# Kernel tuning notes

Measured on AMD Instinct MI355X. Metric: run time of the kernel, lower is better.

Reference implementation:

```python
import jax, jax.numpy as jnp
import numpy as np

B, T_CTX, N_EMBD, N_ATTN, N_HEAD = 8, 1024, 1024, 1024, 16
HEAD_SIZE = N_ATTN // N_HEAD


def _init_time_w():
    # replicates the torch init: per-head exponential decay curves
    curve = np.array([-(T_CTX - 1 - i) for i in range(T_CTX)], dtype=np.float64)
    ww = np.ones((N_HEAD, T_CTX), dtype=np.float32)
    for h in range(N_HEAD):
        if h < N_HEAD - 1:
            decay_speed = T_CTX ** (-(h + 1) / (N_HEAD - 1))
        else:
            decay_speed = 0.0
        ww[h] = np.exp(curve * decay_speed).astype(np.float32)
    return jnp.asarray(ww)


def setup_inputs() -> dict:
    key = jax.random.key(0)
    ks = jax.random.split(key, 6)
    s = 0.02
    return {
        "x": jax.random.normal(ks[0], (B, T_CTX, N_EMBD), jnp.float32),
        "time_w": _init_time_w(),                                   # [H, TT]
        "time_alpha": jnp.ones((N_HEAD, 1, T_CTX), jnp.float32),
        "time_beta": jnp.ones((N_HEAD, T_CTX, 1), jnp.float32),
        "time_gamma": jnp.ones((T_CTX, 1), jnp.float32),
        "Wk": jax.random.normal(ks[1], (N_ATTN, N_EMBD), jnp.float32) * s,
        "bk": jnp.zeros((N_ATTN,), jnp.float32),
        "Wv": jax.random.normal(ks[2], (N_ATTN, N_EMBD), jnp.float32) * s,
        "bv": jnp.zeros((N_ATTN,), jnp.float32),
        "Wr": jax.random.normal(ks[3], (N_ATTN, N_EMBD), jnp.float32) * s,
        "br": jnp.zeros((N_ATTN,), jnp.float32),
        "Wo": jax.random.normal(ks[4], (N_EMBD, N_ATTN), jnp.float32) * s,
        "bo": jnp.zeros((N_EMBD,), jnp.float32),
    }


def _build_w(time_w, time_alpha, time_beta, T):
    # w[h,t,u] = time_w[h, TT-1-(t-u)] for u<=t else 0  (causal decay matrix)
    TT = time_w.shape[1]
    t = jnp.arange(T)[:, None]
    u = jnp.arange(T)[None, :]
    idx = jnp.clip((TT - 1) - t + u, 0, TT - 1)
    mask = u <= t
    w = jnp.where(mask[None, :, :], time_w[:, idx], 0.0)  # [H, T, T]
    return w * time_alpha[:, :, :T] * time_beta[:, :T, :]


def reference(x, time_w, time_alpha, time_beta, time_gamma,
              Wk, bk, Wv, bv, Wr, br, Wo, bo):
    Bb, T, C = x.shape
    H = time_w.shape[0]
    w = _build_w(time_w, time_alpha, time_beta, T)  # [H,T,T]

    # time shift on the first half of channels: prepend zero row, drop last
    x_half = jnp.pad(x[:, :, : C // 2], ((0, 0), (1, 0), (0, 0)))[:, :T, :]
    xs = jnp.concatenate([x_half, x[:, :, C // 2 :]], axis=-1)

    k = xs @ Wk.T + bk
    v = xs @ Wv.T + bv
    r = xs @ Wr.T + br

    k = jnp.exp(jnp.clip(k, -60.0, 30.0))
    sum_k = jnp.cumsum(k, axis=1)  # [B,T,NA]

    kv = (k * v).reshape(Bb, T, H, -1)               # [B,T,H,hs]
    wkv = jnp.einsum('htu,buhc->bthc', w, kv).reshape(Bb, T, -1)

    rwkv = jax.nn.sigmoid(r) * wkv / sum_k
    out = rwkv @ Wo.T + bo
    return out * time_gamma[:T]
```

## Files before the change

kernel.cpp:

```cpp
#include <hip/hip_runtime.h>
#include <hip/hip_bf16.h>
#include <cstddef>
#include <cstdint>

#define B_SZ   8
#define T_CTX  1024
#define C_DIM  1024
#define H_NUM  16
#define HS     64
#define M_ROWS (B_SZ * T_CTX)

typedef __attribute__((ext_vector_type(8))) short bf16x8;
typedef __attribute__((ext_vector_type(8))) unsigned short u16x8;
typedef __attribute__((ext_vector_type(4))) float f32x4;

static __device__ inline unsigned short f2bf(float f) {
    __hip_bfloat16 h = __float2bfloat16(f);
    return __builtin_bit_cast(unsigned short, h);
}
static __device__ inline float bf2f(unsigned short u) {
    unsigned int v = ((unsigned int)u) << 16;
    return __builtin_bit_cast(float, v);
}
static __device__ inline void gld16(const void* g, void* l) {
    __builtin_amdgcn_global_load_lds((const __attribute__((address_space(1))) void*)g,
                                     (__attribute__((address_space(3))) void*)l,
                                     16, 0, 0);
}

__global__ __launch_bounds__(256)
void convert_all(const float* __restrict__ x, unsigned short* __restrict__ xs,
                 const float* __restrict__ Wk, const float* __restrict__ Wv,
                 const float* __restrict__ Wr, const float* __restrict__ Wo,
                 unsigned short* __restrict__ wdst)
{
    const int bid = blockIdx.x;
    if (bid < 8192) {
        const int idx = (bid * 256 + threadIdx.x) * 4;
        const int m = idx >> 10;
        const int c = idx & 1023;
        float4 v;
        if (c < 512) {
            const int t = m & (T_CTX - 1);
            if (t == 0) v = make_float4(0.f, 0.f, 0.f, 0.f);
            else        v = *(const float4*)(x + (size_t)(m - 1) * C_DIM + c);
        } else {
            v = *(const float4*)(x + idx);
        }
        ushort4 o;
        o.x = f2bf(v.x); o.y = f2bf(v.y); o.z = f2bf(v.z); o.w = f2bf(v.w);
        *(ushort4*)(xs + idx) = o;
    } else {
        const int wid = bid - 8192;
        const int z = wid >> 10;
        const float* src = (z == 0) ? Wk : (z == 1) ? Wv : (z == 2) ? Wr : Wo;
        const int idx = ((wid & 1023) * 256 + threadIdx.x) * 4;
        const float4 v = *(const float4*)(src + idx);
        ushort4 o;
        o.x = f2bf(v.x); o.y = f2bf(v.y); o.z = f2bf(v.z); o.w = f2bf(v.w);
        *(ushort4*)(wdst + (size_t)z * (C_DIM * C_DIM) + idx) = o;
    }
}

__global__ __launch_bounds__(256, 2)
void mfma_gemm64(const unsigned short* __restrict__ A,
                 const unsigned short* __restrict__ Wb,
                 const float* __restrict__ b0, const float* __restrict__ b1,
                 const float* __restrict__ b2,
                 void* __restrict__ o0, void* __restrict__ o1, void* __restrict__ o2,
                 const float* __restrict__ gamma, int multi)
{
    const int d  = blockIdx.x;
    const int y  = ((d & 7) << 3) | ((d >> 3) & 7);
    const int xb = d >> 6;
    const int m0 = y * 128, n0 = xb * 128;

    int mode, ncol0;
    const float* bias;
    void* out;
    if (multi) {
        const int z = n0 >> 10;
        mode = z;
        ncol0 = n0 & 1023;
        bias = (z == 0) ? b0 : (z == 1) ? b1 : b2;
        out  = (z == 0) ? o0 : (z == 1) ? o1 : o2;
    } else {
        mode = 3; ncol0 = n0; bias = b0; out = o0;
    }

    __shared__ unsigned short As[128 * 64];
    __shared__ unsigned short Bs[128 * 64];

    const int tid = threadIdx.x;
    const int w = tid >> 6, l = tid & 63;

    const int r8  = l >> 3;
    const int c16 = ((l & 7) ^ r8) * 8;
    const unsigned short* gA = A  + (size_t)(m0 + w * 32 + r8) * C_DIM + c16;
    const unsigned short* gB = Wb + (size_t)(n0 + w * 32 + r8) * C_DIM + c16;
    char* lA = (char*)As + (w * 32) * 128;
    char* lB = (char*)Bs + (w * 32) * 128;

    const int wr = w >> 1, wc = w & 1;
    const int lr = l & 15, lkq = l >> 4;
    const int x7 = lr & 7;

    f32x4 acc[4][4];
    #pragma unroll
    for (int i = 0; i < 4; ++i)
        #pragma unroll
        for (int j = 0; j < 4; ++j) acc[i][j] = (f32x4){0.f, 0.f, 0.f, 0.f};

    for (int k0 = 0; k0 < C_DIM; k0 += 64) {
        #pragma unroll
        for (int r = 0; r < 4; ++r) {
            gld16(gA + k0 + (size_t)r * 8 * C_DIM, lA + r * 8 * 128);
            gld16(gB + k0 + (size_t)r * 8 * C_DIM, lB + r * 8 * 128);
        }
        __syncthreads();

        bf16x8 af[2][4], bfv[2][4];
        #pragma unroll
        for (int ks = 0; ks < 2; ++ks) {
            const int slot = ((ks * 4 + lkq) ^ x7) * 8;
            #pragma unroll
            for (int i = 0; i < 4; ++i)
                af[ks][i] = *(const bf16x8*)&As[(wr * 64 + i * 16 + lr) * 64 + slot];
            #pragma unroll
            for (int j = 0; j < 4; ++j)
                bfv[ks][j] = *(const bf16x8*)&Bs[(wc * 64 + j * 16 + lr) * 64 + slot];
        }
        #pragma unroll
        for (int ks = 0; ks < 2; ++ks)
            #pragma unroll
            for (int i = 0; i < 4; ++i)
                #pragma unroll
                for (int j = 0; j < 4; ++j)
                    acc[i][j] = __builtin_amdgcn_mfma_f32_16x16x32_bf16(
                        af[ks][i], bfv[ks][j], acc[i][j], 0, 0, 0);
        __syncthreads();
    }

    #pragma unroll
    for (int j = 0; j < 4; ++j) {
        const int col = ncol0 + wc * 64 + j * 16 + lr;
        const float bz = bias[col];
        #pragma unroll
        for (int i = 0; i < 4; ++i) {
            const int rb = m0 + wr * 64 + i * 16 + lkq * 4;
            #pragma unroll
            for (int r = 0; r < 4; ++r) {
                const int row = rb + r;
                float v = acc[i][j][r] + bz;
                if (mode == 0)      v = __expf(fminf(fmaxf(v, -60.f), 30.f));
                else if (mode == 2) v = 1.f / (1.f + __expf(-v));
                else if (mode == 3) v *= gamma[row & (T_CTX - 1)];
                if (mode == 1 || mode == 2)
                    ((unsigned short*)out)[(size_t)row * C_DIM + col] = f2bf(v);
                else
                    ((float*)out)[(size_t)row * C_DIM + col] = v;
            }
        }
    }
}

__global__ __launch_bounds__(256)
void cumsum_chunk(const float* __restrict__ expk, const unsigned short* __restrict__ vbf,
                  const float* __restrict__ alpha,
                  float* __restrict__ sumk, unsigned short* __restrict__ kvT,
                  float* __restrict__ aux)
{
    const int n = blockIdx.x * 256 + threadIdx.x;
    const int q = blockIdx.y;
    const int b = blockIdx.z;
    const int h = n >> 6, c = n & 63;
    const size_t base = ((size_t)b * T_CTX + q * 128) * C_DIM + n;
    unsigned short* kvrow = kvT + (((size_t)b * H_NUM + h) * HS + c) * T_CTX + q * 128;
    float s = 0.f;
    u16x8 buf;
    for (int i = 0; i < 128; ++i) {
        const size_t idx = base + (size_t)i * C_DIM;
        const float e  = expk[idx];
        const float vv = bf2f(vbf[idx]);
        const float a  = alpha[h * T_CTX + q * 128 + i];
        s += e;
        sumk[idx] = s;
        buf[i & 7] = f2bf(e * vv * a);
        if ((i & 7) == 7) *(u16x8*)(kvrow + i - 7) = buf;
    }
    aux[((size_t)b * 8 + q) * C_DIM + n] = s;
}

#define REPL_STRIDE 1176
#define REPL_USED   1168

__global__ __launch_bounds__(256)
void wkv_mfma(const unsigned short* __restrict__ kvT,
              const float* __restrict__ sumk,
              const unsigned short* __restrict__ sigr,
              const float* __restrict__ tw, const float* __restrict__ beta,
              const float* __restrict__ aux,
              unsigned short* __restrict__ rwkv)
{
    __shared__ unsigned short repl[8 * REPL_STRIDE];
    __shared__ unsigned short kv_s[64 * 72];
    __shared__ unsigned short tw_s[1024];

    const int tid = threadIdx.x;
    const int bx = blockIdx.x;
    const int t0 = bx * 128;
    const int h  = blockIdx.y;
    const int b  = blockIdx.z;

    {
        const int i = tid * 4;
        const float4 v = *(const float4*)(tw + h * T_CTX + i);
        ushort4 o;
        o.x = f2bf(v.x); o.y = f2bf(v.y); o.z = f2bf(v.z); o.w = f2bf(v.w);
        *(ushort4*)&tw_s[i] = o;
    }
    __syncthreads();

    #pragma unroll
    for (int r = 0; r < 8; ++r)
        for (int i = tid; i < REPL_USED; i += 256) {
            const int src = i + r;
            repl[r * REPL_STRIDE + i] = (src < 1024) ? tw_s[src] : (unsigned short)0;
        }
    __syncthreads();

    const int w = tid >> 6, l = tid & 63;
    const int wr = w >> 1, wc = w & 1;
    const int lr = l & 15, lkq = l >> 4;

    const int r    = (7 - lr) & 7;
    const int S0   = 1023 - t0 - wr * 64 - lr + lkq * 8;
    const int abase = 2 * S0 + (2 * REPL_STRIDE - 2) * r;
    const char* repl_c = (const char*)repl;

    const int srow = tid >> 2;
    const int ucol = (tid & 3) * 16;
    const unsigned short* gkv = kvT + (((size_t)b * H_NUM + h) * HS + srow) * T_CTX + ucol;
    unsigned short* skv = &kv_s[srow * 72 + ucol];

    f32x4 acc[4][2];
    #pragma unroll
    for (int i = 0; i < 4; ++i) {
        acc[i][0] = (f32x4){0.f, 0.f, 0.f, 0.f};
        acc[i][1] = (f32x4){0.f, 0.f, 0.f, 0.f};
    }

    const int nsteps = t0 / 64 + 2;
    for (int ks = 0; ks < nsteps; ++ks) {
        const int u0 = ks * 64;
        const u16x8 q0 = *(const u16x8*)(gkv + u0);
        const u16x8 q1 = *(const u16x8*)(gkv + u0 + 8);
        __syncthreads();
        *(u16x8*)skv       = q0;
        *(u16x8*)(skv + 8) = q1;
        __syncthreads();

        const int ub = abase + 2 * u0;
        #pragma unroll
        for (int kk = 0; kk < 2; ++kk) {
            bf16x8 af[4], bfv[2];
            #pragma unroll
            for (int i = 0; i < 4; ++i)
                af[i] = *(const bf16x8*)(repl_c + (ub + kk * 64 - i * 32));
            #pragma unroll
            for (int j = 0; j < 2; ++j)
                bfv[j] = *(const bf16x8*)&kv_s[(wc * 32 + j * 16 + lr) * 72 + kk * 32 + lkq * 8];
            #pragma unroll
            for (int i = 0; i < 4; ++i)
                #pragma unroll
                for (int j = 0; j < 2; ++j)
                    acc[i][j] = __builtin_amdgcn_mfma_f32_16x16x32_bf16(
                        af[i], bfv[j], acc[i][j], 0, 0, 0);
        }
    }

    float off[2];
    #pragma unroll
    for (int j = 0; j < 2; ++j) {
        const int cl = wc * 32 + j * 16 + lr;
        float o = 0.f;
        for (int q = 0; q < bx; ++q)
            o += aux[((size_t)b * 8 + q) * C_DIM + h * HS + cl];
        off[j] = o;
    }

    #pragma unroll
    for (int i = 0; i < 4; ++i) {
        const int tb = t0 + wr * 64 + i * 16 + lkq * 4;
        #pragma unroll
        for (int rg = 0; rg < 4; ++rg) {
            const int t = tb + rg;
            const float bet = beta[h * T_CTX + t];
            const size_t row_off = ((size_t)(b * T_CTX + t)) * C_DIM + h * HS;
            #pragma unroll
            for (int j = 0; j < 2; ++j) {
                const int cl = wc * 32 + j * 16 + lr;
                const float sk = sumk[row_off + cl] + off[j];
                const float sr = bf2f(sigr[row_off + cl]);
                rwkv[row_off + cl] = f2bf(sr * bet * acc[i][j][rg] / sk);
            }
        }
    }
}

extern "C" void kernel_launch(void* const* d_in, const int* in_sizes, int n_in,
                              void* d_out, int out_size, void* d_ws, size_t ws_size,
                              hipStream_t stream)
{
    const float* x     = (const float*)d_in[0];
    const float* tw    = (const float*)d_in[1];
    const float* alpha = (const float*)d_in[2];
    const float* beta  = (const float*)d_in[3];
    const float* gamma = (const float*)d_in[4];
    const float* Wk    = (const float*)d_in[5];
    const float* bk    = (const float*)d_in[6];
    const float* Wv    = (const float*)d_in[7];
    const float* bv    = (const float*)d_in[8];
    const float* Wr    = (const float*)d_in[9];
    const float* br    = (const float*)d_in[10];
    const float* Wo    = (const float*)d_in[11];
    const float* bo    = (const float*)d_in[12];
    float* out = (float*)d_out;

    char* W = (char*)d_ws;
    float* expk          = (float*)W;
    unsigned short* rwkv = (unsigned short*)W;
    unsigned short* vbf  = (unsigned short*)(W + (32ull << 20));
    unsigned short* wbf  = (unsigned short*)(W + (48ull << 20));
    float* aux           = (float*)(W + (56ull << 20));
    float* sumk          = (float*)(W + (64ull << 20));
    unsigned short* xs   = (unsigned short*)(W + (64ull << 20));
    unsigned short* sigr = (unsigned short*)(W + (96ull << 20));
    unsigned short* kvT  = (unsigned short*)(W + (112ull << 20));

    const size_t WSZ = (size_t)C_DIM * C_DIM;

    convert_all<<<dim3(12288), 256, 0, stream>>>(x, xs, Wk, Wv, Wr, Wo, wbf);

    mfma_gemm64<<<dim3(1536), 256, 0, stream>>>(
        xs, wbf, bk, bv, br, expk, vbf, sigr, gamma, 1);

    cumsum_chunk<<<dim3(4, 8, 8), 256, 0, stream>>>(expk, vbf, alpha, sumk, kvT, aux);

    wkv_mfma<<<dim3(8, 16, 8), 256, 0, stream>>>(
        kvT, sumk, sigr, tw, beta, aux, rwkv);

    mfma_gemm64<<<dim3(512), 256, 0, stream>>>(
        rwkv, wbf + 3 * WSZ, bo, nullptr, nullptr,
        out, nullptr, nullptr, gamma, 0);
}
```

Before: 269.9 us.

## Enlarge GEMM M-tile to 256 rows and halve cumsum chunk length

```diff
diff --git a/kernel.cpp b/kernel.cpp
--- a/kernel.cpp
+++ b/kernel.cpp
@@ -63,17 +63,17 @@
 }
 
 __global__ __launch_bounds__(256, 2)
-void mfma_gemm64(const unsigned short* __restrict__ A,
-                 const unsigned short* __restrict__ Wb,
-                 const float* __restrict__ b0, const float* __restrict__ b1,
-                 const float* __restrict__ b2,
-                 void* __restrict__ o0, void* __restrict__ o1, void* __restrict__ o2,
-                 const float* __restrict__ gamma, int multi)
+void mfma_gemm256(const unsigned short* __restrict__ A,
+                  const unsigned short* __restrict__ Wb,
+                  const float* __restrict__ b0, const float* __restrict__ b1,
+                  const float* __restrict__ b2,
+                  void* __restrict__ o0, void* __restrict__ o1, void* __restrict__ o2,
+                  const float* __restrict__ gamma, int multi)
 {
     const int d  = blockIdx.x;
-    const int y  = ((d & 7) << 3) | ((d >> 3) & 7);
-    const int xb = d >> 6;
-    const int m0 = y * 128, n0 = xb * 128;
+    const int y  = ((d & 7) << 2) | ((d >> 3) & 3);
+    const int xb = d >> 5;
+    const int m0 = y * 256, n0 = xb * 128;
 
     int mode, ncol0;
     const float* bias;
@@ -88,7 +88,7 @@
         mode = 3; ncol0 = n0; bias = b0; out = o0;
     }
 
-    __shared__ unsigned short As[128 * 64];
+    __shared__ unsigned short As[256 * 64];
     __shared__ unsigned short Bs[128 * 64];
 
     const int tid = threadIdx.x;
@@ -96,48 +96,47 @@
 
     const int r8  = l >> 3;
     const int c16 = ((l & 7) ^ r8) * 8;
-    const unsigned short* gA = A  + (size_t)(m0 + w * 32 + r8) * C_DIM + c16;
+    const unsigned short* gA = A  + (size_t)(m0 + w * 64 + r8) * C_DIM + c16;
     const unsigned short* gB = Wb + (size_t)(n0 + w * 32 + r8) * C_DIM + c16;
-    char* lA = (char*)As + (w * 32) * 128;
+    char* lA = (char*)As + (w * 64) * 128;
     char* lB = (char*)Bs + (w * 32) * 128;
 
     const int wr = w >> 1, wc = w & 1;
     const int lr = l & 15, lkq = l >> 4;
     const int x7 = lr & 7;
 
-    f32x4 acc[4][4];
-    #pragma unroll
-    for (int i = 0; i < 4; ++i)
+    f32x4 acc[8][4];
+    #pragma unroll
+    for (int i = 0; i < 8; ++i)
         #pragma unroll
         for (int j = 0; j < 4; ++j) acc[i][j] = (f32x4){0.f, 0.f, 0.f, 0.f};
 
     for (int k0 = 0; k0 < C_DIM; k0 += 64) {
         #pragma unroll
-        for (int r = 0; r < 4; ++r) {
+        for (int r = 0; r < 8; ++r)
             gld16(gA + k0 + (size_t)r * 8 * C_DIM, lA + r * 8 * 128);
+        #pragma unroll
+        for (int r = 0; r < 4; ++r)
             gld16(gB + k0 + (size_t)r * 8 * C_DIM, lB + r * 8 * 128);
-        }
         __syncthreads();
 
-        bf16x8 af[2][4], bfv[2][4];
         #pragma unroll
         for (int ks = 0; ks < 2; ++ks) {
             const int slot = ((ks * 4 + lkq) ^ x7) * 8;
-            #pragma unroll
-            for (int i = 0; i < 4; ++i)
-                af[ks][i] = *(const bf16x8*)&As[(wr * 64 + i * 16 + lr) * 64 + slot];
+            bf16x8 af[8], bfv[4];
+            #pragma unroll
+            for (int i = 0; i < 8; ++i)
+                af[i] = *(const bf16x8*)&As[(wr * 128 + i * 16 + lr) * 64 + slot];
             #pragma unroll
             for (int j = 0; j < 4; ++j)
-                bfv[ks][j] = *(const bf16x8*)&Bs[(wc * 64 + j * 16 + lr) * 64 + slot];
-        }
-        #pragma unroll
-        for (int ks = 0; ks < 2; ++ks)
-            #pragma unroll
-            for (int i = 0; i < 4; ++i)
+                bfv[j] = *(const bf16x8*)&Bs[(wc * 64 + j * 16 + lr) * 64 + slot];
+            #pragma unroll
+            for (int i = 0; i < 8; ++i)
                 #pragma unroll
                 for (int j = 0; j < 4; ++j)
                     acc[i][j] = __builtin_amdgcn_mfma_f32_16x16x32_bf16(
-                        af[ks][i], bfv[ks][j], acc[i][j], 0, 0, 0);
+                        af[i], bfv[j], acc[i][j], 0, 0, 0);
+        }
         __syncthreads();
     }
 
@@ -146,8 +145,8 @@
         const int col = ncol0 + wc * 64 + j * 16 + lr;
         const float bz = bias[col];
         #pragma unroll
-        for (int i = 0; i < 4; ++i) {
-            const int rb = m0 + wr * 64 + i * 16 + lkq * 4;
+        for (int i = 0; i < 8; ++i) {
+            const int rb = m0 + wr * 128 + i * 16 + lkq * 4;
             #pragma unroll
             for (int r = 0; r < 4; ++r) {
                 const int row = rb + r;
@@ -174,21 +173,22 @@
     const int q = blockIdx.y;
     const int b = blockIdx.z;
     const int h = n >> 6, c = n & 63;
-    const size_t base = ((size_t)b * T_CTX + q * 128) * C_DIM + n;
-    unsigned short* kvrow = kvT + (((size_t)b * H_NUM + h) * HS + c) * T_CTX + q * 128;
+    const size_t base = ((size_t)b * T_CTX + q * 64) * C_DIM + n;
+    unsigned short* kvrow = kvT + (((size_t)b * H_NUM + h) * HS + c) * T_CTX + q * 64;
     float s = 0.f;
     u16x8 buf;
-    for (int i = 0; i < 128; ++i) {
+    #pragma unroll 8
+    for (int i = 0; i < 64; ++i) {
         const size_t idx = base + (size_t)i * C_DIM;
         const float e  = expk[idx];
         const float vv = bf2f(vbf[idx]);
-        const float a  = alpha[h * T_CTX + q * 128 + i];
+        const float a  = alpha[h * T_CTX + q * 64 + i];
         s += e;
         sumk[idx] = s;
         buf[i & 7] = f2bf(e * vv * a);
         if ((i & 7) == 7) *(u16x8*)(kvrow + i - 7) = buf;
     }
-    aux[((size_t)b * 8 + q) * C_DIM + n] = s;
+    aux[((size_t)b * 16 + q) * C_DIM + n] = s;
 }
 
 #define REPL_STRIDE 1176
@@ -279,14 +279,15 @@
         }
     }
 
-    float off[2];
+    float off0[2], off1[2];
     #pragma unroll
     for (int j = 0; j < 2; ++j) {
         const int cl = wc * 32 + j * 16 + lr;
         float o = 0.f;
-        for (int q = 0; q < bx; ++q)
-            o += aux[((size_t)b * 8 + q) * C_DIM + h * HS + cl];
-        off[j] = o;
+        for (int q = 0; q < 2 * bx; ++q)
+            o += aux[((size_t)b * 16 + q) * C_DIM + h * HS + cl];
+        off0[j] = o;
+        off1[j] = o + aux[((size_t)b * 16 + 2 * bx) * C_DIM + h * HS + cl];
     }
 
     #pragma unroll
@@ -295,12 +296,13 @@
         #pragma unroll
         for (int rg = 0; rg < 4; ++rg) {
             const int t = tb + rg;
+            const int hi = (t >> 6) & 1;
             const float bet = beta[h * T_CTX + t];
             const size_t row_off = ((size_t)(b * T_CTX + t)) * C_DIM + h * HS;
             #pragma unroll
             for (int j = 0; j < 2; ++j) {
                 const int cl = wc * 32 + j * 16 + lr;
-                const float sk = sumk[row_off + cl] + off[j];
+                const float sk = sumk[row_off + cl] + (hi ? off1[j] : off0[j]);
                 const float sr = bf2f(sigr[row_off + cl]);
                 rwkv[row_off + cl] = f2bf(sr * bet * acc[i][j][rg] / sk);
             }
@@ -342,15 +344,15 @@
 
     convert_all<<<dim3(12288), 256, 0, stream>>>(x, xs, Wk, Wv, Wr, Wo, wbf);
 
-    mfma_gemm64<<<dim3(1536), 256, 0, stream>>>(
+    mfma_gemm256<<<dim3(768), 256, 0, stream>>>(
         xs, wbf, bk, bv, br, expk, vbf, sigr, gamma, 1);
 
-    cumsum_chunk<<<dim3(4, 8, 8), 256, 0, stream>>>(expk, vbf, alpha, sumk, kvT, aux);
+    cumsum_chunk<<<dim3(4, 16, 8), 256, 0, stream>>>(expk, vbf, alpha, sumk, kvT, aux);
 
     wkv_mfma<<<dim3(8, 16, 8), 256, 0, stream>>>(
         kvT, sumk, sigr, tw, beta, aux, rwkv);
 
-    mfma_gemm64<<<dim3(512), 256, 0, stream>>>(
+    mfma_gemm256<<<dim3(256), 256, 0, stream>>>(
         rwkv, wbf + 3 * WSZ, bo, nullptr, nullptr,
         out, nullptr, nullptr, gamma, 0);
 }
```

Result: slower. 308.4 us (+14.3%).

## Shorten cumsum chunks and load wkv K-tiles directly to LDS with swizzle

Applied to the files above, without the earlier changes.

```diff
diff --git a/kernel.cpp b/kernel.cpp
--- a/kernel.cpp
+++ b/kernel.cpp
@@ -174,21 +174,22 @@
     const int q = blockIdx.y;
     const int b = blockIdx.z;
     const int h = n >> 6, c = n & 63;
-    const size_t base = ((size_t)b * T_CTX + q * 128) * C_DIM + n;
-    unsigned short* kvrow = kvT + (((size_t)b * H_NUM + h) * HS + c) * T_CTX + q * 128;
+    const size_t base = ((size_t)b * T_CTX + q * 32) * C_DIM + n;
+    unsigned short* kvrow = kvT + (((size_t)b * H_NUM + h) * HS + c) * T_CTX + q * 32;
     float s = 0.f;
     u16x8 buf;
-    for (int i = 0; i < 128; ++i) {
+    #pragma unroll 8
+    for (int i = 0; i < 32; ++i) {
         const size_t idx = base + (size_t)i * C_DIM;
         const float e  = expk[idx];
         const float vv = bf2f(vbf[idx]);
-        const float a  = alpha[h * T_CTX + q * 128 + i];
+        const float a  = alpha[h * T_CTX + q * 32 + i];
         s += e;
         sumk[idx] = s;
         buf[i & 7] = f2bf(e * vv * a);
         if ((i & 7) == 7) *(u16x8*)(kvrow + i - 7) = buf;
     }
-    aux[((size_t)b * 8 + q) * C_DIM + n] = s;
+    aux[((size_t)b * 32 + q) * C_DIM + n] = s;
 }
 
 #define REPL_STRIDE 1176
@@ -203,7 +204,7 @@
               unsigned short* __restrict__ rwkv)
 {
     __shared__ unsigned short repl[8 * REPL_STRIDE];
-    __shared__ unsigned short kv_s[64 * 72];
+    __shared__ unsigned short kv_s[64 * 128];
     __shared__ unsigned short tw_s[1024];
 
     const int tid = threadIdx.x;
@@ -227,7 +228,6 @@
             const int src = i + r;
             repl[r * REPL_STRIDE + i] = (src < 1024) ? tw_s[src] : (unsigned short)0;
         }
-    __syncthreads();
 
     const int w = tid >> 6, l = tid & 63;
     const int wr = w >> 1, wc = w & 1;
@@ -238,10 +238,11 @@
     const int abase = 2 * S0 + (2 * REPL_STRIDE - 2) * r;
     const char* repl_c = (const char*)repl;
 
-    const int srow = tid >> 2;
-    const int ucol = (tid & 3) * 16;
-    const unsigned short* gkv = kvT + (((size_t)b * H_NUM + h) * HS + srow) * T_CTX + ucol;
-    unsigned short* skv = &kv_s[srow * 72 + ucol];
+    const int rloc = w * 4 + (l >> 4);
+    const int chnk = (l & 15) ^ rloc;
+    const unsigned short* gkv =
+        kvT + (((size_t)b * H_NUM + h) * HS + rloc) * T_CTX + chnk * 8;
+    char* skv = (char*)kv_s + (w * 4) * 256;
 
     f32x4 acc[4][2];
     #pragma unroll
@@ -249,27 +250,27 @@
         acc[i][0] = (f32x4){0.f, 0.f, 0.f, 0.f};
         acc[i][1] = (f32x4){0.f, 0.f, 0.f, 0.f};
     }
-
-    const int nsteps = t0 / 64 + 2;
+    __syncthreads();
+
+    const int nsteps = bx + 1;
     for (int ks = 0; ks < nsteps; ++ks) {
-        const int u0 = ks * 64;
-        const u16x8 q0 = *(const u16x8*)(gkv + u0);
-        const u16x8 q1 = *(const u16x8*)(gkv + u0 + 8);
+        const int u0 = ks * 128;
+        #pragma unroll
+        for (int q = 0; q < 4; ++q)
+            gld16(gkv + (size_t)q * 16 * T_CTX + u0, skv + q * 16 * 256);
         __syncthreads();
-        *(u16x8*)skv       = q0;
-        *(u16x8*)(skv + 8) = q1;
-        __syncthreads();
 
         const int ub = abase + 2 * u0;
         #pragma unroll
-        for (int kk = 0; kk < 2; ++kk) {
+        for (int kk = 0; kk < 4; ++kk) {
             bf16x8 af[4], bfv[2];
             #pragma unroll
             for (int i = 0; i < 4; ++i)
                 af[i] = *(const bf16x8*)(repl_c + (ub + kk * 64 - i * 32));
             #pragma unroll
             for (int j = 0; j < 2; ++j)
-                bfv[j] = *(const bf16x8*)&kv_s[(wc * 32 + j * 16 + lr) * 72 + kk * 32 + lkq * 8];
+                bfv[j] = *(const bf16x8*)&kv_s[(wc * 32 + j * 16 + lr) * 128 +
+                                               (((kk * 4 + lkq) ^ lr) * 8)];
             #pragma unroll
             for (int i = 0; i < 4; ++i)
                 #pragma unroll
@@ -277,16 +278,21 @@
                     acc[i][j] = __builtin_amdgcn_mfma_f32_16x16x32_bf16(
                         af[i], bfv[j], acc[i][j], 0, 0, 0);
         }
-    }
-
-    float off[2];
+        __syncthreads();
+    }
+
+    float off[4][2];
     #pragma unroll
     for (int j = 0; j < 2; ++j) {
         const int cl = wc * 32 + j * 16 + lr;
         float o = 0.f;
-        for (int q = 0; q < bx; ++q)
-            o += aux[((size_t)b * 8 + q) * C_DIM + h * HS + cl];
-        off[j] = o;
+        for (int q = 0; q < 4 * bx; ++q)
+            o += aux[((size_t)b * 32 + q) * C_DIM + h * HS + cl];
+        off[0][j] = o;
+        #pragma unroll
+        for (int s = 1; s < 4; ++s)
+            off[s][j] = off[s - 1][j] +
+                aux[((size_t)b * 32 + 4 * bx + s - 1) * C_DIM + h * HS + cl];
     }
 
     #pragma unroll
@@ -295,12 +301,13 @@
         #pragma unroll
         for (int rg = 0; rg < 4; ++rg) {
             const int t = tb + rg;
+            const int hi = (t >> 5) & 3;
             const float bet = beta[h * T_CTX + t];
             const size_t row_off = ((size_t)(b * T_CTX + t)) * C_DIM + h * HS;
             #pragma unroll
             for (int j = 0; j < 2; ++j) {
                 const int cl = wc * 32 + j * 16 + lr;
-                const float sk = sumk[row_off + cl] + off[j];
+                const float sk = sumk[row_off + cl] + off[hi][j];
                 const float sr = bf2f(sigr[row_off + cl]);
                 rwkv[row_off + cl] = f2bf(sr * bet * acc[i][j][rg] / sk);
             }
@@ -345,7 +352,7 @@
     mfma_gemm64<<<dim3(1536), 256, 0, stream>>>(
         xs, wbf, bk, bv, br, expk, vbf, sigr, gamma, 1);
 
-    cumsum_chunk<<<dim3(4, 8, 8), 256, 0, stream>>>(expk, vbf, alpha, sumk, kvT, aux);
+    cumsum_chunk<<<dim3(4, 32, 8), 256, 0, stream>>>(expk, vbf, alpha, sumk, kvT, aux);
 
     wkv_mfma<<<dim3(8, 16, 8), 256, 0, stream>>>(
         kvT, sumk, sigr, tw, beta, aux, rwkv);
```

Result: slower. 286.8 us (+6.3%).
